# Optimization experiments

Hardware: AMD Instinct MI355X
Metric: run time of the kernel (lower is better)

The kernel has to match this reference:

```python
import jax, jax.numpy as jnp
import numpy as np

HID, NH = 2048, 16
QLR, KVLR = 1536, 512
DR, DN, DQK, DV = 64, 128, 192, 128
S = 2048
EPS = 1e-06


def rmsnorm(x, w, eps=EPS):
    return x * jax.lax.rsqrt(jnp.mean(x * x, axis=-1, keepdims=True) + eps) * w


def rope_interleave(x, cos, sin):
    # x: [B,H,S,D]; cos/sin: [B,S,D] (unsqueezed to head dim 1)
    b, h, s, d = x.shape
    # DeepSeek-V3 interleave: (d//2, 2) -> transpose -> flatten
    x = x.reshape(b, h, s, d // 2, 2).swapaxes(3, 4).reshape(b, h, s, d)
    c = cos[:, None, :, :]
    sn = sin[:, None, :, :]
    x1, x2 = x[..., : d // 2], x[..., d // 2:]
    rot = jnp.concatenate([-x2, x1], axis=-1)
    return x * c + rot * sn


def setup_inputs() -> dict:
    key = jax.random.key(0)
    ks = jax.random.split(key, 8)
    hidden_states = jax.random.normal(ks[0], (1, S, HID), dtype=jnp.float32)
    # real RoPE tables for the 64-dim rope part
    inv_freq = 1.0 / (10000.0 ** (np.arange(0, DR, 2, dtype=np.float32) / DR))
    pos = np.arange(S, dtype=np.float32)
    freqs = pos[:, None] * inv_freq[None, :]          # [S, DR/2]
    emb = np.concatenate([freqs, freqs], axis=-1)     # [S, DR]
    cos = jnp.asarray(np.cos(emb), dtype=jnp.float32)[None]
    sin = jnp.asarray(np.sin(emb), dtype=jnp.float32)[None]
    w = 0.02
    wq_a = jax.random.normal(ks[1], (QLR, HID), dtype=jnp.float32) * w
    q_a_ln_w = jnp.ones((QLR,), dtype=jnp.float32)
    wq_b = jax.random.normal(ks[2], (NH * DQK, QLR), dtype=jnp.float32) * w
    wkv_a = jax.random.normal(ks[3], (KVLR + DR, HID), dtype=jnp.float32) * w
    kv_a_ln_w = jnp.ones((KVLR,), dtype=jnp.float32)
    wkv_b = jax.random.normal(ks[4], (NH * (DN + DV), KVLR), dtype=jnp.float32) * w
    wo = jax.random.normal(ks[5], (HID, NH * DV), dtype=jnp.float32) * w
    cu_seqlens = jnp.array([0, S // 2, S], dtype=jnp.int32)  # two packed docs
    return {"hidden_states": hidden_states, "cos": cos, "sin": sin,
            "wq_a": wq_a, "q_a_ln_w": q_a_ln_w, "wq_b": wq_b,
            "wkv_a": wkv_a, "kv_a_ln_w": kv_a_ln_w, "wkv_b": wkv_b,
            "wo": wo, "cu_seqlens": cu_seqlens, "max_seqlen": S // 2}


def reference(hidden_states, cos, sin, wq_a, q_a_ln_w, wq_b, wkv_a, kv_a_ln_w,
              wkv_b, wo, cu_seqlens, max_seqlen):
    B, s, _ = hidden_states.shape
    # LoRA-compressed Q: q_a -> RMSNorm -> q_b
    q = rmsnorm(hidden_states @ wq_a.T, q_a_ln_w) @ wq_b.T       # [B,S,NH*DQK]
    q = q.reshape(B, s, NH, DQK).transpose(0, 2, 1, 3)           # [B,NH,S,DQK]
    q_pass, q_rot = q[..., :DN], q[..., DN:]
    # compressed KV with MQA rope part
    ckv = hidden_states @ wkv_a.T                                 # [B,S,KVLR+DR]
    kv_c, k_rot = ckv[..., :KVLR], ckv[..., KVLR:]
    kv = rmsnorm(kv_c, kv_a_ln_w) @ wkv_b.T                       # [B,S,NH*(DN+DV)]
    kv = kv.reshape(B, s, NH, DN + DV).transpose(0, 2, 1, 3)      # [B,NH,S,DN+DV]
    k_pass, v = kv[..., :DN], kv[..., DN:]
    k_rot = k_rot[:, None, :, :]                                  # [B,1,S,DR]
    q_rot = rope_interleave(q_rot, cos, sin)
    k_rot = rope_interleave(k_rot, cos, sin)
    k_rot = jnp.broadcast_to(k_rot, (B, NH, s, DR))
    qf = jnp.concatenate([q_pass, q_rot], axis=-1)                # [B,NH,S,DQK]
    kf = jnp.concatenate([k_pass, k_rot], axis=-1)                # [B,NH,S,DQK]
    # varlen causal attention: block-diagonal per document + causal
    pos = jnp.arange(s)
    seg = jnp.searchsorted(cu_seqlens[1:], pos, side='right')
    mask = (seg[:, None] == seg[None, :]) & (pos[:, None] >= pos[None, :])
    scale = DQK ** -0.5  # flash default: 1/sqrt(q head dim) (v padded to DQK)
    scores = jnp.einsum('bhqd,bhkd->bhqk', qf, kf) * scale
    scores = jnp.where(mask[None, None], scores, jnp.finfo(scores.dtype).min)
    attn = jax.nn.softmax(scores, axis=-1)
    out = jnp.einsum('bhqk,bhkd->bhqd', attn, v)                  # [B,NH,S,DV]
    out = out.transpose(0, 2, 1, 3).reshape(B, s, NH * DV)
    return out @ wo.T
```

## Files before the change

kernel.cpp:

```cpp
#include <hip/hip_runtime.h>

typedef unsigned short u16;
typedef __attribute__((ext_vector_type(8))) short bf16x8;
typedef __attribute__((ext_vector_type(4))) float f32x4;

#define HID 2048
#define NH 16
#define QLR 1536
#define KVLR 512
#define DR 64
#define DN 128
#define DQK 192
#define DV 128
#define SEQ 2048
#define NKVA 2176
#define SCALE 0.07216878364870323f

static __device__ __forceinline__ u16 f2bf(float f) {
  unsigned v = __builtin_bit_cast(unsigned, f);
  v = v + 0x7fffu + ((v >> 16) & 1u);
  return (u16)(v >> 16);
}
static __device__ __forceinline__ float bf2f(u16 u) {
  unsigned v = ((unsigned)u) << 16;
  return __builtin_bit_cast(float, v);
}

#define GLOAD16(gp, lp)                                                        \
  __builtin_amdgcn_global_load_lds(                                            \
      (const __attribute__((address_space(1))) void*)(gp),                     \
      (__attribute__((address_space(3))) void*)(lp), 16, 0, 0)

__global__ void k_convert_all(const float* __restrict__ hs, const float* __restrict__ wq_a,
                              const float* __restrict__ wkv_a, const float* __restrict__ wqb,
                              const float* __restrict__ wkvb, const float* __restrict__ wo,
                              u16* __restrict__ hs_bf, u16* __restrict__ wqkva,
                              u16* __restrict__ wqb_bf, u16* __restrict__ wkvb_bf,
                              u16* __restrict__ wo_bf) {
  const long NQ = 4915200;
  long q = (long)blockIdx.x * blockDim.x + threadIdx.x;
  const long stride = (long)gridDim.x * blockDim.x;
  for (; q < NQ; q += stride) {
    const float* src;
    u16* dst;
    long li;
    bool zero = false;
    if (q < 1048576)        { src = hs;   dst = hs_bf;                      li = q; }
    else if (q < 1835008)   { src = wq_a; dst = wqkva;                      li = q - 1048576; }
    else if (q < 2162688)   { li = q - 1835008; src = wkv_a; dst = wqkva + (size_t)QLR * HID;
                              zero = (li >= 294912); }
    else if (q < 3342336)   { src = wqb;  dst = wqb_bf;                     li = q - 2162688; }
    else if (q < 3866624)   { src = wkvb; dst = wkvb_bf;                    li = q - 3342336; }
    else                    { src = wo;   dst = wo_bf;                      li = q - 3866624; }
    u16 o0 = 0, o1 = 0, o2 = 0, o3 = 0;
    if (!zero) {
      const float4 f = *(const float4*)(src + li * 4);
      o0 = f2bf(f.x); o1 = f2bf(f.y); o2 = f2bf(f.z); o3 = f2bf(f.w);
    }
    u16* d = dst + li * 4;
    d[0] = o0; d[1] = o1; d[2] = o2; d[3] = o3;
  }
}

__global__ void k_rmsnorm2(const float* __restrict__ qkva, const float* __restrict__ qw,
                           const float* __restrict__ kvw, u16* __restrict__ q_ln,
                           u16* __restrict__ kv_ln) {
  const int row = blockIdx.x;
  const int which = blockIdx.y;
  const int t = threadIdx.x;
  const int cols = which ? KVLR : QLR;
  const float inv_cols = which ? (1.0f / KVLR) : (1.0f / QLR);
  const float* x = qkva + (size_t)row * NKVA + (which ? QLR : 0);
  const float* w = which ? kvw : qw;
  u16* Y = (which ? kv_ln : q_ln) + (size_t)row * cols;
  float ss = 0.f;
  for (int i = t * 4; i < cols; i += 1024) {
    float4 v = *(const float4*)(x + i);
    ss += v.x * v.x + v.y * v.y + v.z * v.z + v.w * v.w;
  }
#pragma unroll
  for (int m = 1; m < 64; m <<= 1) ss += __shfl_xor(ss, m, 64);
  __shared__ float red[4];
  if ((t & 63) == 0) red[t >> 6] = ss;
  __syncthreads();
  float tot = red[0] + red[1] + red[2] + red[3];
  float r = rsqrtf(tot * inv_cols + 1e-6f);
  for (int i = t * 4; i < cols; i += 1024) {
    float4 v = *(const float4*)(x + i);
    float4 g = *(const float4*)(w + i);
    u16* y = Y + i;
    y[0] = f2bf(v.x * r * g.x);
    y[1] = f2bf(v.y * r * g.y);
    y[2] = f2bf(v.z * r * g.z);
    y[3] = f2bf(v.w * r * g.w);
  }
}

__global__ __launch_bounds__(256) void k_gemm_nt(
    const u16* __restrict__ A, const u16* __restrict__ B, void* __restrict__ Cout,
    int M, int N, int K, int mode) {
  __shared__ __align__(16) u16 As[2][8192];
  __shared__ __align__(16) u16 Bs[2][8192];
  const int t = threadIdx.x;
  const int lane = t & 63;
  const int w = t >> 6, wr = w >> 1, wc = w & 1;
  const int lm = lane & 15, lg = lane >> 4;

  const int nwg = gridDim.x * gridDim.y;
  int bid = blockIdx.y * gridDim.x + blockIdx.x;
  if ((nwg & 7) == 0) bid = (bid & 7) * (nwg >> 3) + (bid >> 3);
  const int bm = bid % gridDim.y;
  const int bn = bid / gridDim.y;

  const int srow = t >> 3;
  const int scol = ((t & 7) ^ (srow & 7)) * 8;
  const u16* aBase = A + (size_t)(bm * 128 + srow) * K + scol;
  const u16* bBase = B + (size_t)(bn * 128 + srow) * K + scol;
  const size_t rowStep = (size_t)32 * K;

#define STAGE(buf, kt_)                                                        \
  do {                                                                         \
    _Pragma("unroll") for (int p = 0; p < 4; ++p) {                            \
      GLOAD16(aBase + (kt_) + p * rowStep, (u16*)As[buf] + p * 2048 + t * 8);  \
      GLOAD16(bBase + (kt_) + p * rowStep, (u16*)Bs[buf] + p * 2048 + t * 8);  \
    }                                                                          \
  } while (0)

  f32x4 acc[4][4] = {};
  const int nk = K >> 6;
  STAGE(0, 0);
  if (nk > 1) STAGE(1, 64);
  int cur = 0;
  for (int kt = 0; kt < nk; ++kt) {
    if (kt + 1 < nk) asm volatile("s_waitcnt vmcnt(8)" ::: "memory");
    else             asm volatile("s_waitcnt vmcnt(0)" ::: "memory");
    __builtin_amdgcn_s_barrier();
    __builtin_amdgcn_sched_barrier(0);
    bf16x8 af[2][4], bfr[2][4];
#pragma unroll
    for (int kk = 0; kk < 2; ++kk) {
#pragma unroll
      for (int i = 0; i < 4; ++i) {
        const int row_ = wr * 64 + i * 16 + lm;
        af[kk][i] = *(const bf16x8*)(As[cur] + row_ * 64 +
                                     ((((kk << 2) | lg) ^ (row_ & 7)) << 3));
      }
#pragma unroll
      for (int j = 0; j < 4; ++j) {
        const int row_ = wc * 64 + j * 16 + lm;
        bfr[kk][j] = *(const bf16x8*)(Bs[cur] + row_ * 64 +
                                      ((((kk << 2) | lg) ^ (row_ & 7)) << 3));
      }
    }
    asm volatile("s_waitcnt lgkmcnt(0)" ::: "memory");
    __builtin_amdgcn_sched_barrier(0);
    __builtin_amdgcn_s_barrier();
    __builtin_amdgcn_sched_barrier(0);
    if (kt + 2 < nk) STAGE(cur, (kt + 2) << 6);
    __builtin_amdgcn_s_setprio(1);
#pragma unroll
    for (int kk = 0; kk < 2; ++kk)
#pragma unroll
      for (int i = 0; i < 4; ++i)
#pragma unroll
        for (int j = 0; j < 4; ++j)
          acc[i][j] = __builtin_amdgcn_mfma_f32_16x16x32_bf16(af[kk][i], bfr[kk][j],
                                                              acc[i][j], 0, 0, 0);
    __builtin_amdgcn_s_setprio(0);
    cur ^= 1;
  }
#undef STAGE

  const int row0 = bm * 128 + wr * 64 + lg * 4;
  const int col0 = bn * 128 + wc * 64 + lm;
  if (mode == 1) {
    u16* C = (u16*)Cout;
#pragma unroll
    for (int i = 0; i < 4; ++i)
#pragma unroll
      for (int r = 0; r < 4; ++r) {
        u16* crow = C + (size_t)(row0 + i * 16 + r) * N + col0;
#pragma unroll
        for (int j = 0; j < 4; ++j) crow[j * 16] = f2bf(acc[i][j][r]);
      }
  } else {
    float* C = (float*)Cout;
#pragma unroll
    for (int i = 0; i < 4; ++i)
#pragma unroll
      for (int r = 0; r < 4; ++r) {
        float* crow = C + (size_t)(row0 + i * 16 + r) * N + col0;
#pragma unroll
        for (int j = 0; j < 4; ++j) crow[j * 16] = acc[i][j][r];
      }
  }
}

template <int WN>
__global__ __launch_bounds__(512) void k_gemm_nt8(
    const u16* __restrict__ A, const u16* __restrict__ B, u16* __restrict__ C,
    int M, int N, int K) {
  constexpr int BN = WN * 64;
  __shared__ __align__(16) u16 As[2][128 * 64];
  __shared__ __align__(16) u16 Bs[2][BN * 64];
  const int t = threadIdx.x;
  const int lane = t & 63;
  const int w = t >> 6, wr = w >> 2, wc = w & 3;
  const int lm = lane & 15, lg = lane >> 4;

  const int nwg = gridDim.x * gridDim.y;
  int bid = blockIdx.y * gridDim.x + blockIdx.x;
  if ((nwg & 7) == 0) bid = (bid & 7) * (nwg >> 3) + (bid >> 3);
  const int bm = bid % gridDim.y;
  const int bn = bid / gridDim.y;

  const u16* aT = A + (size_t)bm * 128 * K;
  const u16* bT = B + (size_t)bn * BN * K;

#define STAGE8(buf, kt_)                                                       \
  do {                                                                         \
    _Pragma("unroll") for (int i = 0; i < 2; ++i) {                            \
      const int g = t + i * 512, row = g >> 3, slot = (g & 7) ^ (row & 7);     \
      GLOAD16(aT + (size_t)row * K + slot * 8 + (kt_), (u16*)As[buf] + g * 8); \
    }                                                                          \
    _Pragma("unroll") for (int i = 0; i < WN; ++i) {                           \
      const int g = t + i * 512, row = g >> 3, slot = (g & 7) ^ (row & 7);     \
      GLOAD16(bT + (size_t)row * K + slot * 8 + (kt_), (u16*)Bs[buf] + g * 8); \
    }                                                                          \
  } while (0)

  f32x4 acc[4][WN] = {};
  const int nk = K >> 6;
  STAGE8(0, 0);
  if (nk > 1) STAGE8(1, 64);
  int cur = 0;
  for (int kt = 0; kt < nk; ++kt) {
    if (kt + 1 < nk) {
      if constexpr (WN == 3) asm volatile("s_waitcnt vmcnt(5)" ::: "memory");
      else                   asm volatile("s_waitcnt vmcnt(6)" ::: "memory");
    } else {
      asm volatile("s_waitcnt vmcnt(0)" ::: "memory");
    }
    __builtin_amdgcn_s_barrier();
    __builtin_amdgcn_sched_barrier(0);
    bf16x8 af[2][4], bfr[2][WN];
#pragma unroll
    for (int kk = 0; kk < 2; ++kk) {
#pragma unroll
      for (int i = 0; i < 4; ++i) {
        const int row_ = wr * 64 + i * 16 + lm;
        af[kk][i] = *(const bf16x8*)(As[cur] + row_ * 64 +
                                     ((((kk << 2) | lg) ^ (row_ & 7)) << 3));
      }
#pragma unroll
      for (int j = 0; j < WN; ++j) {
        const int row_ = wc * (WN * 16) + j * 16 + lm;
        bfr[kk][j] = *(const bf16x8*)(Bs[cur] + row_ * 64 +
                                      ((((kk << 2) | lg) ^ (row_ & 7)) << 3));
      }
    }
    asm volatile("s_waitcnt lgkmcnt(0)" ::: "memory");
    __builtin_amdgcn_sched_barrier(0);
    __builtin_amdgcn_s_barrier();
    __builtin_amdgcn_sched_barrier(0);
    if (kt + 2 < nk) STAGE8(cur, (kt + 2) << 6);
    __builtin_amdgcn_s_setprio(1);
#pragma unroll
    for (int kk = 0; kk < 2; ++kk)
#pragma unroll
      for (int i = 0; i < 4; ++i)
#pragma unroll
        for (int j = 0; j < WN; ++j)
          acc[i][j] = __builtin_amdgcn_mfma_f32_16x16x32_bf16(af[kk][i], bfr[kk][j],
                                                              acc[i][j], 0, 0, 0);
    __builtin_amdgcn_s_setprio(0);
    cur ^= 1;
  }
#undef STAGE8

  const int row0 = bm * 128 + wr * 64 + lg * 4;
  const int col0 = bn * BN + wc * (WN * 16) + lm;
#pragma unroll
  for (int i = 0; i < 4; ++i)
#pragma unroll
    for (int r = 0; r < 4; ++r) {
      u16* crow = C + (size_t)(row0 + i * 16 + r) * N + col0;
#pragma unroll
      for (int j = 0; j < WN; ++j) crow[j * 16] = f2bf(acc[i][j][r]);
    }
}

__global__ void k_mk_qf(const u16* __restrict__ qfull, const float* __restrict__ cosb,
                        const float* __restrict__ sinb, u16* __restrict__ qf) {
  const int s = blockIdx.x, h = blockIdx.y, t = threadIdx.x;
  const u16* src = qfull + (size_t)s * (NH * DQK) + h * DQK;
  u16* dst = qf + ((size_t)h * SEQ + s) * DQK;
  dst[t] = f2bf(bf2f(src[t]) * SCALE);
  if (t < 32) {
    float a = bf2f(src[DN + 2 * t]);
    float b = bf2f(src[DN + 2 * t + 1]);
    float c = cosb[(size_t)s * DR + t];
    float sn = sinb[(size_t)s * DR + t];
    dst[DN + t] = f2bf((a * c - b * sn) * SCALE);
    dst[DN + 32 + t] = f2bf((b * c + a * sn) * SCALE);
  }
}

__global__ __launch_bounds__(256) void k_mk_kf_v(
    const u16* __restrict__ kvfull, const float* __restrict__ krot, int krot_stride,
    const float* __restrict__ cosb, const float* __restrict__ sinb,
    u16* __restrict__ kf, u16* __restrict__ vt) {
  __shared__ u16 vts[128][66];
  const int s0 = blockIdx.x * 64, h = blockIdx.y, t = threadIdx.x;
#pragma unroll
  for (int i = 0; i < 8; ++i) {
    const int g = t + i * 256, row = g >> 5, slot = g & 31;
    const u16* src = kvfull + (size_t)(s0 + row) * (NH * 256) + h * 256 + slot * 8;
    bf16x8 v = *(const bf16x8*)src;
    if (slot < 16) {
      *(bf16x8*)(kf + ((size_t)h * SEQ + s0 + row) * DQK + slot * 8) = v;
    } else {
      const int d = (slot - 16) * 8;
#pragma unroll
      for (int e = 0; e < 8; ++e) vts[d + e][row] = (u16)v[e];
    }
  }
#pragma unroll
  for (int i = 0; i < 8; ++i) {
    const int g = t + i * 256, row = g >> 5, c = g & 31;
    float a = krot[(size_t)(s0 + row) * krot_stride + 2 * c];
    float b = krot[(size_t)(s0 + row) * krot_stride + 2 * c + 1];
    float cc = cosb[(size_t)(s0 + row) * DR + c];
    float sn = sinb[(size_t)(s0 + row) * DR + c];
    u16* kd = kf + ((size_t)h * SEQ + s0 + row) * DQK;
    kd[DN + c] = f2bf(a * cc - b * sn);
    kd[DN + 32 + c] = f2bf(b * cc + a * sn);
  }
  __syncthreads();
#pragma unroll
  for (int i = 0; i < 4; ++i) {
    const int g = t + i * 256, d = g >> 3, slot = g & 7;
    bf16x8 v;
#pragma unroll
    for (int e = 0; e < 8; ++e) v[e] = (short)vts[d][slot * 8 + e];
    *(bf16x8*)(vt + ((size_t)h * DV + d) * SEQ + s0 + slot * 8) = v;
  }
}

__global__ __launch_bounds__(256) void k_attn(
    const u16* __restrict__ qf, const u16* __restrict__ kf, const u16* __restrict__ vt,
    u16* __restrict__ attn_out) {
  __shared__ __align__(16) u16 Ks[2][32 * 192];
  __shared__ __align__(16) u16 Vs[2][128 * 32];
  __shared__ __align__(16) u16 p_lds[4][16][32];

  const int t = threadIdx.x, lane = t & 63, w = t >> 6;
  const int lm = lane & 15, lg = lane >> 4;
  const int bid = blockIdx.x;
  const int x = bid & 7, rr = bid >> 3;
  const int i5 = rr & 31, late = rr >> 5;
  const int tj = late ? (i5 >> 2) : 15 - (i5 >> 2);
  const int h = x * 2 + ((i5 >> 1) & 1);
  const int seg = i5 & 1;
  const int tile_row0 = seg * 1024 + tj * 64;
  const int k_begin = seg * 1024;
  const int n_kt = tj * 2 + 2;

  const int lo_row = tile_row0 + w * 16;
  bf16x8 qfr[6];
  {
    const u16* qp = qf + ((size_t)h * SEQ + (lo_row + lm)) * DQK + lg * 8;
#pragma unroll
    for (int c = 0; c < 6; ++c) qfr[c] = *(const bf16x8*)(qp + c * 32);
  }
  int qrow[4];
#pragma unroll
  for (int r = 0; r < 4; ++r) qrow[r] = lo_row + lg * 4 + r;

  float m_r[4], l_loc[4];
#pragma unroll
  for (int r = 0; r < 4; ++r) { m_r[r] = -3.0e4f; l_loc[r] = 0.f; }
  f32x4 oacc[8] = {};

#define STAGE(buf, kt_)                                                        \
  do {                                                                         \
    const int k0_ = k_begin + (kt_) * 32;                                      \
    _Pragma("unroll") for (int p = 0; p < 3; ++p) {                            \
      const int id = p * 256 + t;                                              \
      const int row = id / 24, colL = id - row * 24;                           \
      const u16* g = kf + ((size_t)h * SEQ + k0_ + row) * DQK +                \
                     ((colL ^ (row & 7)) * 8);                                 \
      GLOAD16(g, (u16*)Ks[buf] + id * 8);                                      \
    }                                                                          \
    _Pragma("unroll") for (int p = 0; p < 2; ++p) {                            \
      const int id = p * 256 + t;                                              \
      const int row = id >> 2, colL = id & 3;                                  \
      const u16* g = vt + ((size_t)h * DV + row) * SEQ + k0_ +                 \
                     ((colL ^ (row & 3)) * 8);                                 \
      GLOAD16(g, (u16*)Vs[buf] + id * 8);                                      \
    }                                                                          \
  } while (0)

#define COMPUTE(buf, kt_)                                                      \
  do {                                                                         \
    const int k0_ = k_begin + (kt_) * 32;                                      \
    f32x4 sc[2] = {};                                                          \
    __builtin_amdgcn_s_setprio(1);                                             \
    _Pragma("unroll") for (int n0_ = 0; n0_ < 2; ++n0_)                        \
        _Pragma("unroll") for (int c_ = 0; c_ < 6; ++c_) {                     \
      const int row_ = n0_ * 16 + lm, cc_ = c_ * 4 + lg;                       \
      bf16x8 kfr = *(const bf16x8*)(Ks[buf] + row_ * 192 +                     \
                                    ((cc_ ^ (row_ & 7)) * 8));                 \
      sc[n0_] = __builtin_amdgcn_mfma_f32_16x16x32_bf16(qfr[c_], kfr,          \
                                                        sc[n0_], 0, 0, 0);     \
    }                                                                          \
    __builtin_amdgcn_s_setprio(0);                                             \
    float s0a[4], s1a[4];                                                      \
    float over = -1e30f;                                                       \
    if (lo_row >= k0_ + 31) {                                                  \
      _Pragma("unroll") for (int r = 0; r < 4; ++r) {                          \
        s0a[r] = sc[0][r];                                                     \
        s1a[r] = sc[1][r];                                                     \
        over = fmaxf(over, fmaxf(s0a[r], s1a[r]) - m_r[r]);                    \
      }                                                                        \
    } else {                                                                   \
      const int kc0 = k0_ + lm, kc1 = k0_ + 16 + lm;                           \
      _Pragma("unroll") for (int r = 0; r < 4; ++r) {                          \
        s0a[r] = (kc0 <= qrow[r]) ? sc[0][r] : -1e30f;                         \
        s1a[r] = (kc1 <= qrow[r]) ? sc[1][r] : -1e30f;                         \
        over = fmaxf(over, fmaxf(s0a[r], s1a[r]) - m_r[r]);                    \
      }                                                                        \
    }                                                                          \
    if (__any(over > 8.0f)) {                                                  \
      _Pragma("unroll") for (int r = 0; r < 4; ++r) {                          \
        float mx = fmaxf(s0a[r], s1a[r]);                                      \
        _Pragma("unroll") for (int md = 1; md < 16; md <<= 1)                  \
            mx = fmaxf(mx, __shfl_xor(mx, md, 64));                            \
        float mnew = fmaxf(m_r[r], mx);                                        \
        float alpha = __expf(m_r[r] - mnew);                                   \
        m_r[r] = mnew;                                                         \
        l_loc[r] *= alpha;                                                     \
        _Pragma("unroll") for (int nd = 0; nd < 8; ++nd) oacc[nd][r] *= alpha; \
      }                                                                        \
    }                                                                          \
    _Pragma("unroll") for (int r = 0; r < 4; ++r) {                            \
      float p0 = __expf(s0a[r] - m_r[r]);                                      \
      float p1 = __expf(s1a[r] - m_r[r]);                                      \
      l_loc[r] += p0 + p1;                                                     \
      p_lds[w][lg * 4 + r][lm] = f2bf(p0);                                     \
      p_lds[w][lg * 4 + r][16 + lm] = f2bf(p1);                                \
    }                                                                          \
    asm volatile("s_waitcnt lgkmcnt(0)" ::: "memory");                         \
    __builtin_amdgcn_sched_barrier(0);                                         \
    bf16x8 pa = *(const bf16x8*)(&p_lds[w][lm][lg * 8]);                       \
    __builtin_amdgcn_s_setprio(1);                                             \
    _Pragma("unroll") for (int nd = 0; nd < 8; ++nd) {                         \
      const int row_ = nd * 16 + lm;                                           \
      bf16x8 vvf = *(const bf16x8*)(Vs[buf] + row_ * 32 +                      \
                                    ((lg ^ (row_ & 3)) * 8));                  \
      oacc[nd] =                                                               \
          __builtin_amdgcn_mfma_f32_16x16x32_bf16(pa, vvf, oacc[nd], 0, 0, 0); \
    }                                                                          \
    __builtin_amdgcn_s_setprio(0);                                             \
  } while (0)

  int cur = 0;
  STAGE(0, 0);
  STAGE(1, 1);
  for (int kt = 0; kt < n_kt; ++kt) {
    if (kt + 1 < n_kt) asm volatile("s_waitcnt vmcnt(5)" ::: "memory");
    else               asm volatile("s_waitcnt vmcnt(0)" ::: "memory");
    __builtin_amdgcn_s_barrier();
    __builtin_amdgcn_sched_barrier(0);
    COMPUTE(cur, kt);
    asm volatile("s_waitcnt lgkmcnt(0)" ::: "memory");
    __builtin_amdgcn_sched_barrier(0);
    __builtin_amdgcn_s_barrier();
    __builtin_amdgcn_sched_barrier(0);
    if (kt + 2 < n_kt) STAGE(cur, kt + 2);
    cur ^= 1;
  }
#undef STAGE
#undef COMPUTE

#pragma unroll
  for (int r = 0; r < 4; ++r) {
    float lt = l_loc[r];
#pragma unroll
    for (int md = 1; md < 16; md <<= 1) lt += __shfl_xor(lt, md, 64);
    float inv = 1.0f / lt;
#pragma unroll
    for (int nd = 0; nd < 8; ++nd)
      attn_out[(size_t)qrow[r] * (NH * DV) + h * DV + nd * 16 + lm] =
          f2bf(oacc[nd][r] * inv);
  }
}

extern "C" void kernel_launch(void* const* d_in, const int* in_sizes, int n_in,
                              void* d_out, int out_size, void* d_ws, size_t ws_size,
                              hipStream_t stream) {
  const float* hs = (const float*)d_in[0];
  const float* cosb = (const float*)d_in[1];
  const float* sinb = (const float*)d_in[2];
  const float* wq_a = (const float*)d_in[3];
  const float* q_a_ln_w = (const float*)d_in[4];
  const float* wq_b = (const float*)d_in[5];
  const float* wkv_a = (const float*)d_in[6];
  const float* kv_a_ln_w = (const float*)d_in[7];
  const float* wkv_b = (const float*)d_in[8];
  const float* wo = (const float*)d_in[9];

  char* ws = (char*)d_ws;
  size_t off = 0;
  auto take = [&](size_t bytes) {
    size_t o = off;
    off += (bytes + 255) & ~(size_t)255;
    return o;
  };
  u16* hs_bf = (u16*)(ws + take((size_t)SEQ * HID * 2));
  u16* wqkva = (u16*)(ws + take((size_t)NKVA * HID * 2));
  u16* wqb = (u16*)(ws + take((size_t)(NH * DQK) * QLR * 2));
  u16* wkvb = (u16*)(ws + take((size_t)(NH * 256) * KVLR * 2));
  u16* wo_bf = (u16*)(ws + take((size_t)HID * (NH * DV) * 2));
  float* qkva = (float*)(ws + take((size_t)SEQ * NKVA * 4));
  u16* q_ln = (u16*)(ws + take((size_t)SEQ * QLR * 2));
  u16* kv_ln = (u16*)(ws + take((size_t)SEQ * KVLR * 2));
  u16* qfull = (u16*)(ws + take((size_t)SEQ * NH * DQK * 2));
  u16* kvfull = (u16*)(ws + take((size_t)SEQ * NH * 256 * 2));
  u16* qf = (u16*)(ws + take((size_t)NH * SEQ * DQK * 2));
  u16* kf = (u16*)(ws + take((size_t)NH * SEQ * DQK * 2));
  u16* vt = (u16*)(ws + take((size_t)NH * DV * SEQ * 2));
  u16* attn = (u16*)(ws + take((size_t)SEQ * NH * DV * 2));
  if (off > ws_size) return;

  k_convert_all<<<2048, 256, 0, stream>>>(hs, wq_a, wkv_a, wq_b, wkv_b, wo,
                                          hs_bf, wqkva, wqb, wkvb, wo_bf);

  dim3 g1(NKVA / 128, SEQ / 128);
  k_gemm_nt<<<g1, 256, 0, stream>>>(hs_bf, wqkva, qkva, SEQ, NKVA, HID, 0);

  k_rmsnorm2<<<dim3(SEQ, 2), 256, 0, stream>>>(qkva, q_a_ln_w, kv_a_ln_w, q_ln, kv_ln);

  dim3 g2(NH * DQK / 192, SEQ / 128);
  k_gemm_nt8<3><<<g2, 512, 0, stream>>>(q_ln, wqb, qfull, SEQ, NH * DQK, QLR);
  dim3 g3(NH * 256 / 256, SEQ / 128);
  k_gemm_nt8<4><<<g3, 512, 0, stream>>>(kv_ln, wkvb, kvfull, SEQ, NH * 256, KVLR);

  k_mk_qf<<<dim3(SEQ, NH), 128, 0, stream>>>(qfull, cosb, sinb, qf);
  k_mk_kf_v<<<dim3(SEQ / 64, NH), 256, 0, stream>>>(kvfull, qkva + (QLR + KVLR), NKVA,
                                                    cosb, sinb, kf, vt);

  k_attn<<<512, 256, 0, stream>>>(qf, kf, vt, attn);

  dim3 g4(HID / 128, SEQ / 128);
  k_gemm_nt<<<g4, 256, 0, stream>>>(attn, wo_bf, d_out, SEQ, HID, NH * DV, 0);
}
```

Baseline: 185.8 us.

## Triple-buffer GEMM and attention loads, fold log2e into Q scale

Both the bf16 GEMM and the attention kernel move from double to triple LDS buffering, with prefetch depth 3 and vmcnt waits adjusted to match. The attention kernel now reads its V fragments into registers before the barrier and issues the PV MFMAs after the next stage is launched, so loads overlap compute. Q is prescaled by log2(e)/sqrt(d), which lets the softmax use exp2f, and the rescale threshold is scaled to match. The extra buffers raise LDS use, which can lower occupancy.

Result: no change. 187.1 us (+0.7%).

```diff
diff --git a/kernel.cpp b/kernel.cpp
--- a/kernel.cpp
+++ b/kernel.cpp
@@ -15,6 +15,8 @@
 #define SEQ 2048
 #define NKVA 2176
 #define SCALE 0.07216878364870323f
+#define SCL2 0.1041164359699839f
+#define THR2 11.541560327111707f
 
 static __device__ __forceinline__ u16 f2bf(float f) {
   unsigned v = __builtin_bit_cast(unsigned, f);
@@ -201,8 +203,9 @@
     const u16* __restrict__ A, const u16* __restrict__ B, u16* __restrict__ C,
     int M, int N, int K) {
   constexpr int BN = WN * 64;
-  __shared__ __align__(16) u16 As[2][128 * 64];
-  __shared__ __align__(16) u16 Bs[2][BN * 64];
+  constexpr int NST = 2 + WN;
+  __shared__ __align__(16) u16 As[3][128 * 64];
+  __shared__ __align__(16) u16 Bs[3][BN * 64];
   const int t = threadIdx.x;
   const int lane = t & 63;
   const int w = t >> 6, wr = w >> 2, wc = w & 3;
@@ -233,14 +236,13 @@
   const int nk = K >> 6;
   STAGE8(0, 0);
   if (nk > 1) STAGE8(1, 64);
-  int cur = 0;
+  if (nk > 2) STAGE8(2, 128);
+  int bt = 0;
   for (int kt = 0; kt < nk; ++kt) {
-    if (kt + 1 < nk) {
-      if constexpr (WN == 3) asm volatile("s_waitcnt vmcnt(5)" ::: "memory");
-      else                   asm volatile("s_waitcnt vmcnt(6)" ::: "memory");
-    } else {
-      asm volatile("s_waitcnt vmcnt(0)" ::: "memory");
-    }
+    const int rem = nk - 1 - kt;
+    if (rem >= 2)      asm volatile("s_waitcnt vmcnt(%0)" :: "i"(2 * NST) : "memory");
+    else if (rem == 1) asm volatile("s_waitcnt vmcnt(%0)" :: "i"(NST) : "memory");
+    else               asm volatile("s_waitcnt vmcnt(0)" ::: "memory");
     __builtin_amdgcn_s_barrier();
     __builtin_amdgcn_sched_barrier(0);
     bf16x8 af[2][4], bfr[2][WN];
@@ -249,13 +251,13 @@
 #pragma unroll
       for (int i = 0; i < 4; ++i) {
         const int row_ = wr * 64 + i * 16 + lm;
-        af[kk][i] = *(const bf16x8*)(As[cur] + row_ * 64 +
+        af[kk][i] = *(const bf16x8*)(As[bt] + row_ * 64 +
                                      ((((kk << 2) | lg) ^ (row_ & 7)) << 3));
       }
 #pragma unroll
       for (int j = 0; j < WN; ++j) {
         const int row_ = wc * (WN * 16) + j * 16 + lm;
-        bfr[kk][j] = *(const bf16x8*)(Bs[cur] + row_ * 64 +
+        bfr[kk][j] = *(const bf16x8*)(Bs[bt] + row_ * 64 +
                                       ((((kk << 2) | lg) ^ (row_ & 7)) << 3));
       }
     }
@@ -263,7 +265,7 @@
     __builtin_amdgcn_sched_barrier(0);
     __builtin_amdgcn_s_barrier();
     __builtin_amdgcn_sched_barrier(0);
-    if (kt + 2 < nk) STAGE8(cur, (kt + 2) << 6);
+    if (kt + 3 < nk) STAGE8(bt, (kt + 3) << 6);
     __builtin_amdgcn_s_setprio(1);
 #pragma unroll
     for (int kk = 0; kk < 2; ++kk)
@@ -274,7 +276,7 @@
           acc[i][j] = __builtin_amdgcn_mfma_f32_16x16x32_bf16(af[kk][i], bfr[kk][j],
                                                               acc[i][j], 0, 0, 0);
     __builtin_amdgcn_s_setprio(0);
-    cur ^= 1;
+    bt = (bt == 2) ? 0 : bt + 1;
   }
 #undef STAGE8
 
@@ -295,14 +297,14 @@
   const int s = blockIdx.x, h = blockIdx.y, t = threadIdx.x;
   const u16* src = qfull + (size_t)s * (NH * DQK) + h * DQK;
   u16* dst = qf + ((size_t)h * SEQ + s) * DQK;
-  dst[t] = f2bf(bf2f(src[t]) * SCALE);
+  dst[t] = f2bf(bf2f(src[t]) * SCL2);
   if (t < 32) {
     float a = bf2f(src[DN + 2 * t]);
     float b = bf2f(src[DN + 2 * t + 1]);
     float c = cosb[(size_t)s * DR + t];
     float sn = sinb[(size_t)s * DR + t];
-    dst[DN + t] = f2bf((a * c - b * sn) * SCALE);
-    dst[DN + 32 + t] = f2bf((b * c + a * sn) * SCALE);
+    dst[DN + t] = f2bf((a * c - b * sn) * SCL2);
+    dst[DN + 32 + t] = f2bf((b * c + a * sn) * SCL2);
   }
 }
 
@@ -350,8 +352,8 @@
 __global__ __launch_bounds__(256) void k_attn(
     const u16* __restrict__ qf, const u16* __restrict__ kf, const u16* __restrict__ vt,
     u16* __restrict__ attn_out) {
-  __shared__ __align__(16) u16 Ks[2][32 * 192];
-  __shared__ __align__(16) u16 Vs[2][128 * 32];
+  __shared__ __align__(16) u16 Ks[3][32 * 192];
+  __shared__ __align__(16) u16 Vs[3][128 * 32];
   __shared__ __align__(16) u16 p_lds[4][16][32];
 
   const int t = threadIdx.x, lane = t & 63, w = t >> 6;
@@ -381,6 +383,7 @@
 #pragma unroll
   for (int r = 0; r < 4; ++r) { m_r[r] = -3.0e4f; l_loc[r] = 0.f; }
   f32x4 oacc[8] = {};
+  bf16x8 pa, vv[8];
 
 #define STAGE(buf, kt_)                                                        \
   do {                                                                         \
@@ -401,7 +404,7 @@
     }                                                                          \
   } while (0)
 
-#define COMPUTE(buf, kt_)                                                      \
+#define COMPUTE1(buf, kt_)                                                     \
   do {                                                                         \
     const int k0_ = k_begin + (kt_) * 32;                                      \
     f32x4 sc[2] = {};                                                          \
@@ -431,57 +434,61 @@
         over = fmaxf(over, fmaxf(s0a[r], s1a[r]) - m_r[r]);                    \
       }                                                                        \
     }                                                                          \
-    if (__any(over > 8.0f)) {                                                  \
+    if (__any(over > THR2)) {                                                  \
       _Pragma("unroll") for (int r = 0; r < 4; ++r) {                          \
         float mx = fmaxf(s0a[r], s1a[r]);                                      \
         _Pragma("unroll") for (int md = 1; md < 16; md <<= 1)                  \
             mx = fmaxf(mx, __shfl_xor(mx, md, 64));                            \
         float mnew = fmaxf(m_r[r], mx);                                        \
-        float alpha = __expf(m_r[r] - mnew);                                   \
+        float alpha = exp2f(m_r[r] - mnew);                                    \
         m_r[r] = mnew;                                                         \
         l_loc[r] *= alpha;                                                     \
         _Pragma("unroll") for (int nd = 0; nd < 8; ++nd) oacc[nd][r] *= alpha; \
       }                                                                        \
     }                                                                          \
     _Pragma("unroll") for (int r = 0; r < 4; ++r) {                            \
-      float p0 = __expf(s0a[r] - m_r[r]);                                      \
-      float p1 = __expf(s1a[r] - m_r[r]);                                      \
+      float p0 = exp2f(s0a[r] - m_r[r]);                                       \
+      float p1 = exp2f(s1a[r] - m_r[r]);                                       \
       l_loc[r] += p0 + p1;                                                     \
       p_lds[w][lg * 4 + r][lm] = f2bf(p0);                                     \
       p_lds[w][lg * 4 + r][16 + lm] = f2bf(p1);                                \
     }                                                                          \
     asm volatile("s_waitcnt lgkmcnt(0)" ::: "memory");                         \
     __builtin_amdgcn_sched_barrier(0);                                         \
-    bf16x8 pa = *(const bf16x8*)(&p_lds[w][lm][lg * 8]);                       \
-    __builtin_amdgcn_s_setprio(1);                                             \
+    pa = *(const bf16x8*)(&p_lds[w][lm][lg * 8]);                              \
     _Pragma("unroll") for (int nd = 0; nd < 8; ++nd) {                         \
       const int row_ = nd * 16 + lm;                                           \
-      bf16x8 vvf = *(const bf16x8*)(Vs[buf] + row_ * 32 +                      \
-                                    ((lg ^ (row_ & 3)) * 8));                  \
-      oacc[nd] =                                                               \
-          __builtin_amdgcn_mfma_f32_16x16x32_bf16(pa, vvf, oacc[nd], 0, 0, 0); \
-    }                                                                          \
-    __builtin_amdgcn_s_setprio(0);                                             \
+      vv[nd] = *(const bf16x8*)(Vs[buf] + row_ * 32 +                          \
+                                ((lg ^ (row_ & 3)) * 8));                      \
+    }                                                                          \
   } while (0)
 
-  int cur = 0;
   STAGE(0, 0);
   STAGE(1, 1);
+  if (n_kt > 2) STAGE(2, 2);
+  int bt = 0;
   for (int kt = 0; kt < n_kt; ++kt) {
-    if (kt + 1 < n_kt) asm volatile("s_waitcnt vmcnt(5)" ::: "memory");
+    const int rem = n_kt - 1 - kt;
+    if (rem >= 2)      asm volatile("s_waitcnt vmcnt(10)" ::: "memory");
+    else if (rem == 1) asm volatile("s_waitcnt vmcnt(5)" ::: "memory");
     else               asm volatile("s_waitcnt vmcnt(0)" ::: "memory");
     __builtin_amdgcn_s_barrier();
     __builtin_amdgcn_sched_barrier(0);
-    COMPUTE(cur, kt);
+    COMPUTE1(bt, kt);
     asm volatile("s_waitcnt lgkmcnt(0)" ::: "memory");
     __builtin_amdgcn_sched_barrier(0);
     __builtin_amdgcn_s_barrier();
     __builtin_amdgcn_sched_barrier(0);
-    if (kt + 2 < n_kt) STAGE(cur, kt + 2);
-    cur ^= 1;
+    if (kt + 3 < n_kt) STAGE(bt, kt + 3);
+    __builtin_amdgcn_s_setprio(1);
+#pragma unroll
+    for (int nd = 0; nd < 8; ++nd)
+      oacc[nd] = __builtin_amdgcn_mfma_f32_16x16x32_bf16(pa, vv[nd], oacc[nd], 0, 0, 0);
+    __builtin_amdgcn_s_setprio(0);
+    bt = (bt == 2) ? 0 : bt + 1;
   }
 #undef STAGE
-#undef COMPUTE
+#undef COMPUTE1
 
 #pragma unroll
   for (int r = 0; r < 4; ++r) {
```
